# Kernel optimization log

Hardware: AMD Instinct MI355X
Metric: run time of the kernel (lower is better)

## Reference

```python
import jax, jax.numpy as jnp
import numpy as np

P = 4   # patch_size
H = 8   # num_heads


def setup_inputs() -> dict:
    key = jax.random.key(0)
    k0, k1, k2 = jax.random.split(key, 3)
    B, C, R = 8, 8, 64
    E = C * P ** 3  # 512
    s = 1.0 / np.sqrt(E)
    x = jax.random.normal(k0, (B, C, R, R, R), jnp.float32)
    in_proj_w = jax.random.normal(k1, (3 * E, E), jnp.float32) * s
    in_proj_b = jnp.zeros((3 * E,), jnp.float32)
    out_proj_w = jax.random.normal(k2, (E, E), jnp.float32) * s
    out_proj_b = jnp.zeros((E,), jnp.float32)
    return {"x": x, "in_proj_w": in_proj_w, "in_proj_b": in_proj_b,
            "out_proj_w": out_proj_w, "out_proj_b": out_proj_b}


def reference(x, in_proj_w, in_proj_b, out_proj_w, out_proj_b):
    B, C, Rx, Ry, Rz = x.shape
    p = P
    nx, ny, nz = Rx // p, Ry // p, Rz // p
    N = nx * ny * nz
    E = C * p ** 3
    dh = E // H

    # cyclic shift: move last patch to front == roll by +p on each spatial axis
    x = jnp.roll(x, (p, p, p), axis=(2, 3, 4))

    # window partition: (B,C,nx,p,ny,p,nz,p) -> (B, N, C*p^3), matching
    # unfold + flatten + permute + flatten of the torch code
    xw = (x.reshape(B, C, nx, p, ny, p, nz, p)
           .transpose(0, 2, 4, 6, 1, 3, 5, 7)
           .reshape(B, N, E))

    # nn.MultiheadAttention with batch_first=False: seq dim = B, batch dim = N
    qkv = jnp.einsum('bne,fe->bnf', xw, in_proj_w) + in_proj_b  # (B, N, 3E)
    q, k, v = jnp.split(qkv, 3, axis=-1)
    q = q.reshape(B, N, H, dh)
    k = k.reshape(B, N, H, dh)
    v = v.reshape(B, N, H, dh)
    scale = 1.0 / np.sqrt(dh)
    # attention over the B (sequence) axis, independently per window n and head h
    att = jax.nn.softmax(jnp.einsum('inhd,jnhd->nhij', q * scale, k), axis=-1)
    o = jnp.einsum('nhij,jnhd->inhd', att, v).reshape(B, N, E)
    o = jnp.einsum('bne,fe->bnf', o, out_proj_w) + out_proj_b  # (B, N, E)

    # torch reassembly via the cat-of-permute loops interleaves windows:
    # out[b, c, px*nx + ix, py*ny + iy, pz*nz + iz] = y[b, ix, iy, iz, c, px, py, pz]
    y = (o.reshape(B, nx, ny, nz, C, p, p, p)
          .transpose(0, 4, 5, 1, 6, 2, 7, 3)
          .reshape(B, C, Rx, Ry, Rz))

    # reverse cyclic shift: roll by -p on each spatial axis
    y = jnp.roll(y, (-p, -p, -p), axis=(2, 3, 4))
    return y
```

## Files before the change

### kernel.cpp

```cpp
#include <hip/hip_runtime.h>

typedef unsigned short u16;
typedef unsigned int u32;
typedef __bf16 bf16x8 __attribute__((ext_vector_type(8)));
typedef float f32x4 __attribute__((ext_vector_type(4)));
typedef unsigned short u16x8 __attribute__((ext_vector_type(8)));

__device__ __forceinline__ u16 f2bf(float f) {
  u32 u = __builtin_bit_cast(u32, f);
  u = (u + 0x7FFFu + ((u >> 16) & 1u)) >> 16;
  return (u16)u;
}
__device__ __forceinline__ float bf2f(u16 h) {
  u32 u = ((u32)h) << 16;
  return __builtin_bit_cast(float, u);
}

#define GLD16(gp, lp) __builtin_amdgcn_global_load_lds( \
    (const __attribute__((address_space(1))) u32*)(const void*)(gp), \
    (__attribute__((address_space(3))) u32*)(void*)(lp), 16, 0, 0)
#define SBAR() __builtin_amdgcn_s_barrier()
#define SCHED0() __builtin_amdgcn_sched_barrier(0)

__global__ __launch_bounds__(256) void cast_f32_bf16(const float* __restrict__ src,
                                                     u16* __restrict__ dst, int n4) {
  int i = blockIdx.x * 256 + threadIdx.x;
  if (i < n4) {
    float4 v = *(const float4*)(src + (size_t)i * 4);
    ushort4 u;
    u.x = f2bf(v.x); u.y = f2bf(v.y); u.z = f2bf(v.z); u.w = f2bf(v.w);
    *(ushort4*)(dst + (size_t)i * 4) = u;
  }
}

__global__ __launch_bounds__(256) void permute_in(const float* __restrict__ x,
                                                  u16* __restrict__ xw) {
  __shared__ float lds[128 * 64];
  int t = threadIdx.x;
  int bx = blockIdx.x;
  int b = blockIdx.y;
  int jx = bx >> 4, jy = bx & 15;
#pragma unroll
  for (int it = 0; it < 8; ++it) {
    int idx = t + it * 256;
    int row = idx >> 4, z4 = idx & 15;
    int c = row >> 4, qx = (row >> 2) & 3, qy = row & 3;
    int X = (jx * 4 + qx + 60) & 63;
    int Y = (jy * 4 + qy + 60) & 63;
    float4 v = *(const float4*)(x + ((((size_t)(b * 8 + c) * 64 + X) * 64 + Y) * 64 + z4 * 4));
    *(float4*)(lds + row * 64 + ((z4 ^ (row & 7)) << 2)) = v;
  }
  __syncthreads();
#pragma unroll
  for (int it = 0; it < 8; ++it) {
    int idx = t + it * 256;
    int jz = idx >> 7, r = idx & 127;
    int z4r = (jz + 15) & 15;
    float4 v = *(const float4*)(lds + r * 64 + ((z4r ^ (r & 7)) << 2));
    int nw = jx * 256 + jy * 16 + jz;
    ushort4 u;
    u.x = f2bf(v.x); u.y = f2bf(v.y); u.z = f2bf(v.z); u.w = f2bf(v.w);
    *(ushort4*)(xw + (size_t)(nw * 8 + b) * 512 + r * 4) = u;
  }
}

__global__ __launch_bounds__(512, 1) void gemm_qkv_attn(const u16* __restrict__ A,
                                                        const u16* __restrict__ W,
                                                        const float* __restrict__ bias,
                                                        u16* __restrict__ O) {
  __shared__ u16 smem[57344];
  u16* As = smem;
  u16* Bs = smem + 32768;

  int cpx = gridDim.x >> 3;
  int wg = (blockIdx.x & 7) * cpx + (blockIdx.x >> 3);
  int mb = wg >> 3, h = wg & 7;
  int m0 = mb * 256;

  int tid = threadIdx.x;
  int w = tid >> 6, l = tid & 63;
  int wr = w >> 2, wc = w & 3;
  int lr = l & 15, lg = l >> 4;

  const u16* pa[4]; int dA[4];
#pragma unroll
  for (int i = 0; i < 4; ++i) {
    int slot = w * 256 + i * 64 + l;
    int row = slot >> 3, kg = (slot & 7) ^ (row & 7);
    pa[i] = A + (size_t)(m0 + row) * 512 + kg * 8;
    dA[i] = (w * 256 + i * 64) * 8;
  }
  const u16* pb[3]; int dB[3];
#pragma unroll
  for (int i = 0; i < 3; ++i) {
    int slot = w * 192 + i * 64 + l;
    int row = slot >> 3, kg = (slot & 7) ^ (row & 7);
    int grow = (row >> 6) * 512 + h * 64 + (row & 63);
    pb[i] = W + (size_t)grow * 512 + kg * 8;
    dB[i] = (w * 192 + i * 64) * 8;
  }

  int cx0 = lg ^ (lr & 7), cx1 = cx0 ^ 4;
  int aofs[2] = { (wr * 128 + lr) * 64 + cx0 * 8, (wr * 128 + lr) * 64 + cx1 * 8 };
  int bofs[2] = { (wc * 48 + lr) * 64 + cx0 * 8, (wc * 48 + lr) * 64 + cx1 * 8 };

  f32x4 acc[8][3] = {};

#pragma unroll
  for (int i = 0; i < 4; ++i) GLD16(pa[i], As + dA[i]);
#pragma unroll
  for (int i = 0; i < 3; ++i) GLD16(pb[i], Bs + dB[i]);
  asm volatile("s_waitcnt vmcnt(0)" ::: "memory");
  SCHED0(); SBAR(); SCHED0();

  for (int t = 0; t < 8; ++t) {
    const u16* AsT = As + (t & 1) * 16384;
    const u16* BsT = Bs + (t & 1) * 12288;
    u16* Ad = As + ((t + 1) & 1) * 16384;
    u16* Bd = Bs + ((t + 1) & 1) * 12288;
    int nx = (t + 1) * 64;
    bool st = (t < 7);
    bf16x8 bfr[3][2];
#pragma unroll
    for (int pg = 0; pg < 4; ++pg) {
      bf16x8 afr[2][2];
#pragma unroll
      for (int mi = 0; mi < 2; ++mi)
#pragma unroll
        for (int kk = 0; kk < 2; ++kk)
          afr[mi][kk] = *(const bf16x8*)(AsT + aofs[kk] + (pg * 2 + mi) * 1024);
      if (pg == 0) {
#pragma unroll
        for (int n = 0; n < 3; ++n)
#pragma unroll
          for (int kk = 0; kk < 2; ++kk)
            bfr[n][kk] = *(const bf16x8*)(BsT + bofs[kk] + n * 1024);
      }
      if (pg == 0 && st) { GLD16(pa[0] + nx, Ad + dA[0]); GLD16(pa[1] + nx, Ad + dA[1]); }
      if (pg == 1 && st) { GLD16(pa[2] + nx, Ad + dA[2]); GLD16(pa[3] + nx, Ad + dA[3]); }
      if (pg == 2 && st) { GLD16(pb[0] + nx, Bd + dB[0]); GLD16(pb[1] + nx, Bd + dB[1]); }
      if (pg == 3 && st) { GLD16(pb[2] + nx, Bd + dB[2]); }
      SCHED0();
      __builtin_amdgcn_s_setprio(1);
#pragma unroll
      for (int mi = 0; mi < 2; ++mi)
#pragma unroll
        for (int n = 0; n < 3; ++n)
#pragma unroll
          for (int kk = 0; kk < 2; ++kk)
            acc[pg * 2 + mi][n] =
                __builtin_amdgcn_mfma_f32_16x16x32_bf16(bfr[n][kk], afr[mi][kk],
                                                        acc[pg * 2 + mi][n], 0, 0, 0);
      __builtin_amdgcn_s_setprio(0);
      SCHED0();
    }
    asm volatile("s_waitcnt vmcnt(0)" ::: "memory");
    SCHED0(); SBAR(); SCHED0();
  }

  u16* ct = smem;
#pragma unroll
  for (int n = 0; n < 3; ++n) {
    int col0 = wc * 48 + n * 16 + lg * 4;
    int gcol = ((col0 >> 6) << 9) + (h << 6) + (col0 & 63);
    float4 bv = *(const float4*)(bias + gcol);
#pragma unroll
    for (int m = 0; m < 8; ++m) {
      int row = wr * 128 + m * 16 + lr;
      ushort4 uu;
      uu.x = f2bf(acc[m][n][0] + bv.x);
      uu.y = f2bf(acc[m][n][1] + bv.y);
      uu.z = f2bf(acc[m][n][2] + bv.z);
      uu.w = f2bf(acc[m][n][3] + bv.w);
      *(ushort4*)(ct + row * 200 + col0) = uu;
    }
  }
  __syncthreads();

  int nw2 = tid >> 4, u4 = tid & 15, qi = u4 >> 1, jh = u4 & 1;
  const u16* qrow = ct + (nw2 * 8 + qi) * 200;
  float s4[4];
#pragma unroll
  for (int jj = 0; jj < 4; ++jj) {
    const u16* kr = ct + (nw2 * 8 + jh * 4 + jj) * 200 + 64;
    float sacc = 0.f;
#pragma unroll
    for (int dc = 0; dc < 8; ++dc) {
      u16x8 qv = *(const u16x8*)(qrow + dc * 8);
      u16x8 kv = *(const u16x8*)(kr + dc * 8);
#pragma unroll
      for (int e = 0; e < 8; ++e)
        sacc += bf2f((u16)qv[e]) * bf2f((u16)kv[e]);
    }
    s4[jj] = sacc * 0.125f;
  }
  float r0 = __shfl_xor(s4[0], 1), r1 = __shfl_xor(s4[1], 1);
  float r2 = __shfl_xor(s4[2], 1), r3 = __shfl_xor(s4[3], 1);
  float sm[8];
  if (jh == 0) {
    sm[0] = s4[0]; sm[1] = s4[1]; sm[2] = s4[2]; sm[3] = s4[3];
    sm[4] = r0; sm[5] = r1; sm[6] = r2; sm[7] = r3;
  } else {
    sm[0] = r0; sm[1] = r1; sm[2] = r2; sm[3] = r3;
    sm[4] = s4[0]; sm[5] = s4[1]; sm[6] = s4[2]; sm[7] = s4[3];
  }
  float mx = sm[0];
#pragma unroll
  for (int j = 1; j < 8; ++j) mx = fmaxf(mx, sm[j]);
  float p[8], psum = 0.f;
#pragma unroll
  for (int j = 0; j < 8; ++j) { p[j] = __expf(sm[j] - mx); psum += p[j]; }
  float inv = 1.f / psum;

  float ov[32];
#pragma unroll
  for (int e = 0; e < 32; ++e) ov[e] = 0.f;
#pragma unroll
  for (int j = 0; j < 8; ++j) {
    const u16* vr = ct + (nw2 * 8 + j) * 200 + 128 + jh * 32;
    float pj = p[j] * inv;
#pragma unroll
    for (int dc = 0; dc < 4; ++dc) {
      u16x8 vv = *(const u16x8*)(vr + dc * 8);
#pragma unroll
      for (int e = 0; e < 8; ++e)
        ov[dc * 8 + e] += pj * bf2f((u16)vv[e]);
    }
  }
  u32 pk[16];
#pragma unroll
  for (int e = 0; e < 16; ++e)
    pk[e] = (u32)f2bf(ov[2 * e]) | ((u32)f2bf(ov[2 * e + 1]) << 16);
  u32* dst = (u32*)(O + (size_t)(m0 + nw2 * 8 + qi) * 512 + h * 64 + jh * 32);
#pragma unroll
  for (int q4 = 0; q4 < 4; ++q4) {
    uint4 vq; vq.x = pk[q4 * 4]; vq.y = pk[q4 * 4 + 1];
    vq.z = pk[q4 * 4 + 2]; vq.w = pk[q4 * 4 + 3];
    *(uint4*)(dst + q4 * 4) = vq;
  }
}

__global__ __launch_bounds__(512, 1) void gemm_out(const u16* __restrict__ A,
                                                   const u16* __restrict__ W,
                                                   const float* __restrict__ bias,
                                                   u16* __restrict__ C) {
  __shared__ u16 smem[65536];
  u16* As = smem;
  u16* Bs = smem + 32768;

  int cpx = gridDim.x >> 3;
  int wg = (blockIdx.x & 7) * cpx + (blockIdx.x >> 3);
  int mb = wg >> 1, nb = wg & 1;
  int m0 = mb * 256, n0 = nb * 256;

  int tid = threadIdx.x;
  int w = tid >> 6, l = tid & 63;
  int wr = w >> 2, wc = w & 3;
  int lr = l & 15, lg = l >> 4;

  const u16* pa[4]; const u16* pb[4]; int dS[4];
#pragma unroll
  for (int i = 0; i < 4; ++i) {
    int slot = w * 256 + i * 64 + l;
    int row = slot >> 3, kg = (slot & 7) ^ (row & 7);
    pa[i] = A + (size_t)(m0 + row) * 512 + kg * 8;
    pb[i] = W + (size_t)(n0 + row) * 512 + kg * 8;
    dS[i] = (w * 256 + i * 64) * 8;
  }

  int cx0 = lg ^ (lr & 7), cx1 = cx0 ^ 4;
  int aofs[2] = { (wr * 128 + lr) * 64 + cx0 * 8, (wr * 128 + lr) * 64 + cx1 * 8 };
  int bofs[2] = { (wc * 64 + lr) * 64 + cx0 * 8, (wc * 64 + lr) * 64 + cx1 * 8 };

  f32x4 acc[8][4] = {};

#pragma unroll
  for (int i = 0; i < 4; ++i) GLD16(pa[i], As + dS[i]);
#pragma unroll
  for (int i = 0; i < 4; ++i) GLD16(pb[i], Bs + dS[i]);
  asm volatile("s_waitcnt vmcnt(0)" ::: "memory");
  SCHED0(); SBAR(); SCHED0();

  for (int t = 0; t < 8; ++t) {
    const u16* AsT = As + (t & 1) * 16384;
    const u16* BsT = Bs + (t & 1) * 16384;
    u16* Ad = As + ((t + 1) & 1) * 16384;
    u16* Bd = Bs + ((t + 1) & 1) * 16384;
    int nx = (t + 1) * 64;
    bool st = (t < 7);
    bf16x8 bfr[4][2];
#pragma unroll
    for (int pg = 0; pg < 4; ++pg) {
      bf16x8 afr[2][2];
#pragma unroll
      for (int mi = 0; mi < 2; ++mi)
#pragma unroll
        for (int kk = 0; kk < 2; ++kk)
          afr[mi][kk] = *(const bf16x8*)(AsT + aofs[kk] + (pg * 2 + mi) * 1024);
      if (pg == 0) {
#pragma unroll
        for (int n = 0; n < 4; ++n)
#pragma unroll
          for (int kk = 0; kk < 2; ++kk)
            bfr[n][kk] = *(const bf16x8*)(BsT + bofs[kk] + n * 1024);
      }
      if (pg == 0 && st) { GLD16(pa[0] + nx, Ad + dS[0]); GLD16(pa[1] + nx, Ad + dS[1]); }
      if (pg == 1 && st) { GLD16(pa[2] + nx, Ad + dS[2]); GLD16(pa[3] + nx, Ad + dS[3]); }
      if (pg == 2 && st) { GLD16(pb[0] + nx, Bd + dS[0]); GLD16(pb[1] + nx, Bd + dS[1]); }
      if (pg == 3 && st) { GLD16(pb[2] + nx, Bd + dS[2]); GLD16(pb[3] + nx, Bd + dS[3]); }
      SCHED0();
      __builtin_amdgcn_s_setprio(1);
#pragma unroll
      for (int mi = 0; mi < 2; ++mi)
#pragma unroll
        for (int n = 0; n < 4; ++n)
#pragma unroll
          for (int kk = 0; kk < 2; ++kk)
            acc[pg * 2 + mi][n] =
                __builtin_amdgcn_mfma_f32_16x16x32_bf16(bfr[n][kk], afr[mi][kk],
                                                        acc[pg * 2 + mi][n], 0, 0, 0);
      __builtin_amdgcn_s_setprio(0);
      SCHED0();
    }
    asm volatile("s_waitcnt vmcnt(0)" ::: "memory");
    SCHED0(); SBAR(); SCHED0();
  }

#pragma unroll
  for (int n = 0; n < 4; ++n) {
    int col0 = n0 + wc * 64 + n * 16 + lg * 4;
    float4 bv = *(const float4*)(bias + col0);
#pragma unroll
    for (int m = 0; m < 8; ++m) {
      size_t row = (size_t)(m0 + wr * 128 + m * 16 + lr);
      ushort4 uu;
      uu.x = f2bf(acc[m][n][0] + bv.x);
      uu.y = f2bf(acc[m][n][1] + bv.y);
      uu.z = f2bf(acc[m][n][2] + bv.z);
      uu.w = f2bf(acc[m][n][3] + bv.w);
      *(ushort4*)(C + row * 512 + col0) = uu;
    }
  }
}

__global__ __launch_bounds__(256) void permute_out(const u16* __restrict__ o2,
                                                   float* __restrict__ out) {
  __shared__ float lds[16 * 516];
  int t = threadIdx.x;
  int bx = blockIdx.x;
  int b = blockIdx.y;
  int ix = bx >> 4, iy = bx & 15;
  int n0 = ix * 256 + iy * 16;
#pragma unroll
  for (int it = 0; it < 8; ++it) {
    int idx = t + it * 256;
    int iz = idx >> 7, fq = idx & 127;
    ushort4 u = *(const ushort4*)(o2 + ((size_t)((n0 + iz) * 8 + b) * 512 + fq * 4));
    float4 v;
    v.x = bf2f(u.x); v.y = bf2f(u.y); v.z = bf2f(u.z); v.w = bf2f(u.w);
    *(float4*)(lds + iz * 516 + fq * 4) = v;
  }
  __syncthreads();
#pragma unroll
  for (int it = 0; it < 8; ++it) {
    int idx = t + it * 256;
    int fidx = idx >> 4, w4 = idx & 15;
    int c = fidx >> 4, px = (fidx >> 2) & 3, py = fidx & 3;
    int W0 = (w4 * 4 + 4) & 63;
    int pz = W0 >> 4, iz0 = W0 & 15;
    int fa = fidx * 4 + pz;
    float4 v;
    v.x = lds[(iz0 + 0) * 516 + fa];
    v.y = lds[(iz0 + 1) * 516 + fa];
    v.z = lds[(iz0 + 2) * 516 + fa];
    v.w = lds[(iz0 + 3) * 516 + fa];
    int uu = (px * 16 + ix + 60) & 63;
    int vv = (py * 16 + iy + 60) & 63;
    *(float4*)(out + ((((size_t)(b * 8 + c) * 64 + uu) * 64 + vv) * 64 + w4 * 4)) = v;
  }
}

extern "C" void kernel_launch(void* const* d_in, const int* in_sizes, int n_in,
                              void* d_out, int out_size, void* d_ws, size_t ws_size,
                              hipStream_t stream) {
  const float* x     = (const float*)d_in[0];
  const float* w_in  = (const float*)d_in[1];
  const float* b_in  = (const float*)d_in[2];
  const float* w_out = (const float*)d_in[3];
  const float* b_out = (const float*)d_in[4];
  float* out = (float*)d_out;

  char* ws = (char*)d_ws;
  u16* wq  = (u16*)(ws);
  u16* wo  = (u16*)(ws + 1572864);
  u16* xw2 = (u16*)(ws + 2097152);
  u16* o   = (u16*)(ws + 35651584);
  u16* o2  = (u16*)(ws + 69206016);

  cast_f32_bf16<<<768, 256, 0, stream>>>(w_in, wq, 196608);
  cast_f32_bf16<<<256, 256, 0, stream>>>(w_out, wo, 65536);
  permute_in<<<dim3(256, 8), 256, 0, stream>>>(x, xw2);
  gemm_qkv_attn<<<1024, 512, 0, stream>>>(xw2, wq, b_in, o);
  gemm_out<<<256, 512, 0, stream>>>(o, wo, b_out, o2);
  permute_out<<<dim3(256, 8), 256, 0, stream>>>(o2, out);
}
```

Before: 144.4 us.

## Fuse output permutation into out-projection GEMM epilogue and merge weight casts

```diff
diff --git a/kernel.cpp b/kernel.cpp
--- a/kernel.cpp
+++ b/kernel.cpp
@@ -22,15 +22,17 @@
 #define SBAR() __builtin_amdgcn_s_barrier()
 #define SCHED0() __builtin_amdgcn_sched_barrier(0)
 
-__global__ __launch_bounds__(256) void cast_f32_bf16(const float* __restrict__ src,
-                                                     u16* __restrict__ dst, int n4) {
+__global__ __launch_bounds__(256) void cast_both(const float* __restrict__ w_in,
+                                                 u16* __restrict__ wq,
+                                                 const float* __restrict__ w_out,
+                                                 u16* __restrict__ wo) {
   int i = blockIdx.x * 256 + threadIdx.x;
-  if (i < n4) {
-    float4 v = *(const float4*)(src + (size_t)i * 4);
-    ushort4 u;
-    u.x = f2bf(v.x); u.y = f2bf(v.y); u.z = f2bf(v.z); u.w = f2bf(v.w);
-    *(ushort4*)(dst + (size_t)i * 4) = u;
-  }
+  const float* src = w_in; u16* dst = wq; int idx = i;
+  if (i >= 196608) { src = w_out; dst = wo; idx = i - 196608; }
+  float4 v = *(const float4*)(src + (size_t)idx * 4);
+  ushort4 u;
+  u.x = f2bf(v.x); u.y = f2bf(v.y); u.z = f2bf(v.z); u.w = f2bf(v.w);
+  *(ushort4*)(dst + (size_t)idx * 4) = u;
 }
 
 __global__ __launch_bounds__(256) void permute_in(const float* __restrict__ x,
@@ -240,13 +242,14 @@
   }
 }
 
-__global__ __launch_bounds__(512, 1) void gemm_out(const u16* __restrict__ A,
-                                                   const u16* __restrict__ W,
-                                                   const float* __restrict__ bias,
-                                                   u16* __restrict__ C) {
+__global__ __launch_bounds__(512, 1) void gemm_out_fused(const u16* __restrict__ A,
+                                                         const u16* __restrict__ W,
+                                                         const float* __restrict__ bias,
+                                                         float* __restrict__ outp) {
   __shared__ u16 smem[65536];
   u16* As = smem;
   u16* Bs = smem + 32768;
+  float* ldsT = (float*)smem;
 
   int cpx = gridDim.x >> 3;
   int wg = (blockIdx.x & 7) * cpx + (blockIdx.x >> 3);
@@ -326,57 +329,56 @@
     SCHED0(); SBAR(); SCHED0();
   }
 
-#pragma unroll
-  for (int n = 0; n < 4; ++n) {
-    int col0 = n0 + wc * 64 + n * 16 + lg * 4;
-    float4 bv = *(const float4*)(bias + col0);
-#pragma unroll
-    for (int m = 0; m < 8; ++m) {
-      size_t row = (size_t)(m0 + wr * 128 + m * 16 + lr);
-      ushort4 uu;
-      uu.x = f2bf(acc[m][n][0] + bv.x);
-      uu.y = f2bf(acc[m][n][1] + bv.y);
-      uu.z = f2bf(acc[m][n][2] + bv.z);
-      uu.w = f2bf(acc[m][n][3] + bv.w);
-      *(ushort4*)(C + row * 512 + col0) = uu;
-    }
-  }
-}
-
-__global__ __launch_bounds__(256) void permute_out(const u16* __restrict__ o2,
-                                                   float* __restrict__ out) {
-  __shared__ float lds[16 * 516];
-  int t = threadIdx.x;
-  int bx = blockIdx.x;
-  int b = blockIdx.y;
-  int ix = bx >> 4, iy = bx & 15;
-  int n0 = ix * 256 + iy * 16;
-#pragma unroll
-  for (int it = 0; it < 8; ++it) {
-    int idx = t + it * 256;
-    int iz = idx >> 7, fq = idx & 127;
-    ushort4 u = *(const ushort4*)(o2 + ((size_t)((n0 + iz) * 8 + b) * 512 + fq * 4));
-    float4 v;
-    v.x = bf2f(u.x); v.y = bf2f(u.y); v.z = bf2f(u.z); v.w = bf2f(u.w);
-    *(float4*)(lds + iz * 516 + fq * 4) = v;
-  }
   __syncthreads();
-#pragma unroll
-  for (int it = 0; it < 8; ++it) {
-    int idx = t + it * 256;
-    int fidx = idx >> 4, w4 = idx & 15;
-    int c = fidx >> 4, px = (fidx >> 2) & 3, py = fidx & 3;
-    int W0 = (w4 * 4 + 4) & 63;
-    int pz = W0 >> 4, iz0 = W0 & 15;
-    int fa = fidx * 4 + pz;
-    float4 v;
-    v.x = lds[(iz0 + 0) * 516 + fa];
-    v.y = lds[(iz0 + 1) * 516 + fa];
-    v.z = lds[(iz0 + 2) * 516 + fa];
-    v.w = lds[(iz0 + 3) * 516 + fa];
-    int uu = (px * 16 + ix + 60) & 63;
-    int vv = (py * 16 + iy + 60) & 63;
-    *(float4*)(out + ((((size_t)(b * 8 + c) * 64 + uu) * 64 + vv) * 64 + w4 * 4)) = v;
+
+  float4 bvv[4];
+#pragma unroll
+  for (int n = 0; n < 4; ++n)
+    bvv[n] = *(const float4*)(bias + n0 + wc * 64 + n * 16 + lg * 4);
+
+  int ix = mb >> 3;
+  int iy0 = (mb * 2) & 15;
+  int jhalf = lr >> 3;
+
+#pragma unroll 1
+  for (int b = 0; b < 8; ++b) {
+    if ((lr & 7) == b) {
+#pragma unroll
+      for (int m = 0; m < 8; ++m) {
+        int j = wr * 16 + m * 2 + jhalf;
+#pragma unroll
+        for (int n = 0; n < 4; ++n) {
+          int col0 = wc * 64 + n * 16 + lg * 4;
+          float4 stv;
+          stv.x = acc[m][n][0] + bvv[n].x;
+          stv.y = acc[m][n][1] + bvv[n].y;
+          stv.z = acc[m][n][2] + bvv[n].z;
+          stv.w = acc[m][n][3] + bvv[n].w;
+          *(float4*)(ldsT + j * 260 + col0) = stv;
+        }
+      }
+    }
+    __syncthreads();
+#pragma unroll
+    for (int it = 0; it < 4; ++it) {
+      int idx = tid + it * 512;
+      int w4 = idx & 15, iyr = (idx >> 4) & 1, fl = idx >> 5;
+      int cl = fl >> 4, px = (fl >> 2) & 3, py = fl & 3;
+      int W0 = (w4 * 4 + 4) & 63;
+      int pz = W0 >> 4, iz0 = W0 & 15;
+      int fa = fl * 4 + pz;
+      int rbase = iyr * 16 + iz0;
+      float4 v;
+      v.x = ldsT[(rbase + 0) * 260 + fa];
+      v.y = ldsT[(rbase + 1) * 260 + fa];
+      v.z = ldsT[(rbase + 2) * 260 + fa];
+      v.w = ldsT[(rbase + 3) * 260 + fa];
+      int c = nb * 4 + cl;
+      int uu = (px * 16 + ix + 60) & 63;
+      int vv = (py * 16 + iy0 + iyr + 60) & 63;
+      *(float4*)(outp + ((((size_t)(b * 8 + c) * 64 + uu) * 64 + vv) * 64 + w4 * 4)) = v;
+    }
+    __syncthreads();
   }
 }
 
@@ -395,12 +397,9 @@
   u16* wo  = (u16*)(ws + 1572864);
   u16* xw2 = (u16*)(ws + 2097152);
   u16* o   = (u16*)(ws + 35651584);
-  u16* o2  = (u16*)(ws + 69206016);
-
-  cast_f32_bf16<<<768, 256, 0, stream>>>(w_in, wq, 196608);
-  cast_f32_bf16<<<256, 256, 0, stream>>>(w_out, wo, 65536);
+
+  cast_both<<<1024, 256, 0, stream>>>(w_in, wq, w_out, wo);
   permute_in<<<dim3(256, 8), 256, 0, stream>>>(x, xw2);
   gemm_qkv_attn<<<1024, 512, 0, stream>>>(xw2, wq, b_in, o);
-  gemm_out<<<256, 512, 0, stream>>>(o, wo, b_out, o2);
-  permute_out<<<dim3(256, 8), 256, 0, stream>>>(o2, out);
-}
+  gemm_out_fused<<<256, 512, 0, stream>>>(o, wo, b_out, out);
+}
```

After: 132.9 us. -8.0%, faster.
